# Kernel optimization log

Hardware: AMD Instinct MI355X
Metric: run time of the kernel (lower is better)

## Reference

```python
import jax, jax.numpy as jnp
import numpy as np

B, S, H, F, E, TOPK = 2, 2048, 1024, 512, 8, 2


def setup_inputs() -> dict:
    key = jax.random.key(0)
    k1, k2, k3, k4, k5 = jax.random.split(key, 5)
    s_h = 1.0 / np.sqrt(H)
    s_f = 1.0 / np.sqrt(F)
    return {
        "x": jax.random.normal(k1, (B, S, H), dtype=jnp.float32),
        "Wr": jax.random.normal(k2, (H, E), dtype=jnp.float32) * s_h,   # router
        "Wg": jax.random.normal(k3, (E, H, F), dtype=jnp.float32) * s_h,  # gate proj
        "Wu": jax.random.normal(k4, (E, H, F), dtype=jnp.float32) * s_h,  # up proj
        "Wd": jax.random.normal(k5, (E, F, H), dtype=jnp.float32) * s_f,  # down proj
        "topk": TOPK,
    }


def reference(x, Wr, Wg, Wu, Wd, topk):
    Bq, Sq, Hq = x.shape
    Eq = Wr.shape[1]
    xf = x.reshape(-1, Hq)                      # [T, H]
    logits = xf @ Wr                            # [T, E]
    probs = jax.nn.softmax(logits, axis=-1)
    w, idx = jax.lax.top_k(probs, topk)         # [T, topk]
    w = w / jnp.sum(w, axis=-1, keepdims=True)  # normalize top-k probs (Qwen3-style)
    # combine coefficients per (token, expert): scatter top-k weights
    coeff = jnp.sum(jax.nn.one_hot(idx, Eq, dtype=w.dtype) * w[..., None], axis=1)  # [T, E]
    # dense dispatch/combine (math-equivalent to per-expert gather + scatter-add)
    gate = jnp.einsum('th,ehf->tef', xf, Wg)    # [T, E, F]
    up = jnp.einsum('th,ehf->tef', xf, Wu)
    act = jax.nn.silu(gate) * up                # SwiGLU expert
    # apply combine weight before down-proj (linearity) to avoid a [T,E,H] temp
    out = jnp.einsum('tef,efh->th', act * coeff[:, :, None], Wd)
    return out.reshape(Bq, Sq, Hq)
```

## Files before the change

### kernel.cpp

```cpp
#include <hip/hip_runtime.h>
#include <hip/hip_bf16.h>

#define T_TOK    4096
#define H_DIM    1024
#define F_DIM    512
#define N_EXP    8
#define N_ASSIGN 8192
#define BM 128
#define BN 128
#define BK 64
#define MAX_TILES 80
#define GRID_MT   71
#define TRU      3072

typedef __bf16 bf16x8 __attribute__((ext_vector_type(8)));
typedef float  f32x4  __attribute__((ext_vector_type(4)));

#define MFMA16(a, b, c) __builtin_amdgcn_mfma_f32_16x16x32_bf16((a), (b), (c), 0, 0, 0)

__device__ __forceinline__ void gl_lds16(const __bf16* g, __bf16* l) {
    __builtin_amdgcn_global_load_lds(
        (const __attribute__((address_space(1))) unsigned int*)g,
        (__attribute__((address_space(3))) unsigned int*)l,
        16, 0, 0);
}

__global__ __launch_bounds__(256) void transpose_kernel(
    const float* __restrict__ Wg, const float* __restrict__ Wu, const float* __restrict__ Wd,
    __bf16* __restrict__ Wcat, __bf16* __restrict__ Wdt)
{
    __shared__ float tile[64][65];
    int b = blockIdx.x, tid = threadIdx.x;
    const float* src; int C, z, c0, r0;
    if (b < 2048) {
        z = b >> 7; int rem = b & 127;
        c0 = (rem & 7) * 64; r0 = (rem >> 3) * 64;
        src = (z < 8) ? Wg + (size_t)z * H_DIM * F_DIM
                      : Wu + (size_t)(z - 8) * H_DIM * F_DIM;
        C = F_DIM;
    } else {
        int v = b - 2048; z = 16 + (v >> 7); int rem = v & 127;
        c0 = (rem & 15) * 64; r0 = (rem >> 4) * 64;
        src = Wd + (size_t)(z - 16) * F_DIM * H_DIM;
        C = H_DIM;
    }
    int fr = tid >> 4, f4 = tid & 15;
#pragma unroll
    for (int p = 0; p < 4; ++p) {
        int row = p * 16 + fr;
        float4 v = *(const float4*)(src + (size_t)(r0 + row) * C + c0 + f4 * 4);
        tile[row][f4 * 4 + 0] = v.x; tile[row][f4 * 4 + 1] = v.y;
        tile[row][f4 * 4 + 2] = v.z; tile[row][f4 * 4 + 3] = v.w;
    }
    __syncthreads();
    int j = tid & 7, cl = tid >> 3;
#pragma unroll
    for (int p = 0; p < 2; ++p) {
        int c = cl + p * 32;
        bf16x8 v;
#pragma unroll
        for (int i = 0; i < 8; ++i) v[i] = (__bf16)tile[8 * j + i][c];
        if (z < 16) {
            int e = (z < 8) ? z : z - 8;
            int sel = (z < 8) ? 0 : 16;
            int f = c0 + c;
            int pp = ((f >> 4) << 5) + (f & 15) + sel;
            *(bf16x8*)&Wcat[(size_t)e * 2 * F_DIM * H_DIM + (size_t)pp * H_DIM + r0 + 8 * j] = v;
        } else {
            *(bf16x8*)&Wdt[(size_t)(z - 16) * H_DIM * F_DIM + (size_t)(c0 + c) * F_DIM + r0 + 8 * j] = v;
        }
    }
}

__global__ __launch_bounds__(256) void routing_kernel(
    const float* __restrict__ x, const float* __restrict__ Wr,
    __bf16* __restrict__ xb, int* __restrict__ top_e, float* __restrict__ top_w)
{
    __shared__ float WrS[N_EXP * H_DIM];
    int tid = threadIdx.x;
    for (int i = tid; i < N_EXP * H_DIM; i += 256) {
        int h = i >> 3, e = i & 7;
        WrS[e * H_DIM + (h ^ (e << 2))] = Wr[i];
    }
    __syncthreads();

    int wave = tid >> 6, lane = tid & 63;
    int t = blockIdx.x * 4 + wave;
    const float* xrow = x + (size_t)t * H_DIM;
    __bf16* xbrow = xb + (size_t)t * H_DIM;

    float part[N_EXP];
#pragma unroll
    for (int e = 0; e < N_EXP; ++e) part[e] = 0.f;
#pragma unroll 4
    for (int s = 0; s < 16; ++s) {
        int h = s * 64 + lane;
        float xs = xrow[h];
        xbrow[h] = (__bf16)xs;
#pragma unroll
        for (int e = 0; e < N_EXP; ++e) part[e] += xs * WrS[e * H_DIM + (h ^ (e << 2))];
    }
#pragma unroll
    for (int m = 1; m < 64; m <<= 1) {
#pragma unroll
        for (int e = 0; e < N_EXP; ++e) part[e] += __shfl_xor(part[e], m, 64);
    }
    if (lane == 0) {
        float v1 = -1e30f, v2 = -1e30f;
        int i1 = 0, i2 = 0;
#pragma unroll
        for (int e = 0; e < N_EXP; ++e) {
            float p = part[e];
            if (p > v1)      { v2 = v1; i2 = i1; v1 = p; i1 = e; }
            else if (p > v2) { v2 = p;  i2 = e; }
        }
        float w1 = 1.f / (1.f + __expf(v2 - v1));
        top_e[t * 2]     = i1;  top_e[t * 2 + 1] = i2;
        top_w[t * 2]     = w1;  top_w[t * 2 + 1] = 1.f - w1;
    }
}

__global__ __launch_bounds__(256) void sort_kernel(
    const int* __restrict__ top_e, const float* __restrict__ top_w,
    int* __restrict__ perm, float* __restrict__ wts, int* __restrict__ tokslot,
    int* __restrict__ tile_e, int* __restrict__ tile_m0, int* __restrict__ tile_cnt,
    int* __restrict__ n_tiles)
{
    __shared__ int hist[N_EXP][256];
    __shared__ int ebase[N_EXP];
    int tid = threadIdx.x, myexp = blockIdx.x;
    int c[N_EXP];
#pragma unroll
    for (int e = 0; e < N_EXP; ++e) c[e] = 0;
#pragma unroll 4
    for (int i = 0; i < 32; ++i) {
        int ee = top_e[i * 256 + tid];
#pragma unroll
        for (int e = 0; e < N_EXP; ++e) c[e] += (ee == e);
    }
#pragma unroll
    for (int e = 0; e < N_EXP; ++e) hist[e][tid] = c[e];
    __syncthreads();
    for (int s = 1; s < 256; s <<= 1) {
        int v[N_EXP];
#pragma unroll
        for (int e = 0; e < N_EXP; ++e) v[e] = (tid >= s) ? hist[e][tid - s] : 0;
        __syncthreads();
#pragma unroll
        for (int e = 0; e < N_EXP; ++e) hist[e][tid] += v[e];
        __syncthreads();
    }
    if (tid == 0) {
        int o = 0, nt = 0;
        for (int e = 0; e < N_EXP; ++e) {
            ebase[e] = o;
            int ne = hist[e][255];
            if (myexp == 0) {
                for (int m0 = 0; m0 < ne; m0 += BM) {
                    tile_e[nt]   = e;
                    tile_m0[nt]  = o + m0;
                    tile_cnt[nt] = (ne - m0 < BM) ? (ne - m0) : BM;
                    ++nt;
                }
            }
            o += ne;
        }
        if (myexp == 0) *n_tiles = nt;
    }
    __syncthreads();
    int base = ebase[myexp] + hist[myexp][tid] - c[myexp];
#pragma unroll 4
    for (int i = 0; i < 32; ++i) {
        int a = i * 256 + tid;
        if (top_e[a] == myexp) {
            perm[base]   = a >> 1;
            wts[base]    = top_w[a];
            tokslot[a]   = base;
            ++base;
        }
    }
}

__global__ __launch_bounds__(256, 3) void gateup_kernel(
    const __bf16* __restrict__ xb, const __bf16* __restrict__ Wcat,
    const int* __restrict__ perm, const float* __restrict__ wts,
    const int* __restrict__ tile_e, const int* __restrict__ tile_m0, const int* __restrict__ tile_cnt,
    const int* __restrict__ n_tiles, __bf16* __restrict__ act)
{
    int nat = (blockIdx.x & 7) * GRID_MT + (blockIdx.x >> 3);
    int mt = nat >> 3;
    if (mt >= *n_tiles) return;
    int e = tile_e[mt], m0 = tile_m0[mt], mcnt = tile_cnt[mt];
    int n0 = (nat & 7) * BN;
    __shared__ __align__(16) __bf16 As[BM * BK];
    __shared__ __align__(16) __bf16 Bs[BN * BK];
    __shared__ int   rowtok[BM];
    __shared__ float roww[BM];
    int tid = threadIdx.x;
    if (tid < BM) {
        int slot = m0 + ((tid < mcnt) ? tid : 0);
        rowtok[tid] = perm[slot];
        roww[tid]   = wts[slot];
    }
    __syncthreads();
    int wave = tid >> 6, lane = tid & 63;
    int srow   = wave * 8 + (lane >> 3);
    int schunk = (((lane & 7) ^ ((lane >> 3) & 7))) * 8;
    const __bf16* We = Wcat + (size_t)e * (2 * F_DIM) * H_DIM;
    const __bf16* aptr[4];
    const __bf16* bptr[4];
#pragma unroll
    for (int j = 0; j < 4; ++j) {
        int r = j * 32 + srow;
        aptr[j] = xb + (size_t)rowtok[r] * H_DIM + schunk;
        bptr[j] = We + (size_t)(n0 + r) * H_DIM + schunk;
    }
    __bf16* aLds = As + wave * 512;
    __bf16* bLds = Bs + wave * 512;
    int wm = wave & 1, wn = wave >> 1;
    int quad = lane >> 4, l16 = lane & 15;
    f32x4 acc[4][4];
#pragma unroll
    for (int a = 0; a < 4; ++a)
#pragma unroll
        for (int b = 0; b < 4; ++b) acc[a][b] = (f32x4){0.f, 0.f, 0.f, 0.f};
    for (int k0 = 0; k0 < H_DIM; k0 += BK) {
#pragma unroll
        for (int j = 0; j < 4; ++j) {
            gl_lds16(aptr[j] + k0, aLds + j * 2048);
            gl_lds16(bptr[j] + k0, bLds + j * 2048);
        }
        __syncthreads();
#pragma unroll
        for (int s = 0; s < 2; ++s) {
            int sw = (((quad + s * 4) ^ (l16 & 7))) * 8;
            bf16x8 af[4], bf[4];
#pragma unroll
            for (int im = 0; im < 4; ++im)
                af[im] = *(const bf16x8*)&As[(wm * 64 + im * 16 + l16) * 64 + sw];
#pragma unroll
            for (int in = 0; in < 4; ++in)
                bf[in] = *(const bf16x8*)&Bs[(wn * 64 + in * 16 + l16) * 64 + sw];
#pragma unroll
            for (int im = 0; im < 4; ++im)
#pragma unroll
                for (int in = 0; in < 4; ++in)
                    acc[im][in] = MFMA16(af[im], bf[in], acc[im][in]);
        }
        __syncthreads();
    }
    int fbase = (n0 >> 1) + wn * 32;
#pragma unroll
    for (int im = 0; im < 4; ++im) {
#pragma unroll
        for (int ip = 0; ip < 2; ++ip) {
            f32x4 g = acc[im][ip * 2], u = acc[im][ip * 2 + 1];
            int fcol = fbase + ip * 16 + l16;
#pragma unroll
            for (int r = 0; r < 4; ++r) {
                int rl = wm * 64 + im * 16 + quad * 4 + r;
                if (rl < mcnt) {
                    float gv = g[r], uv = u[r];
                    float sg = gv / (1.f + __expf(-gv));
                    act[(size_t)(m0 + rl) * F_DIM + fcol] = (__bf16)(sg * uv * roww[rl]);
                }
            }
        }
    }
}

__global__ __launch_bounds__(256, 3) void down_kernel(
    const __bf16* __restrict__ act, const __bf16* __restrict__ Wdt,
    const int* __restrict__ tile_e, const int* __restrict__ tile_m0, const int* __restrict__ tile_cnt,
    const int* __restrict__ n_tiles, __bf16* __restrict__ P)
{
    int nat = (blockIdx.x & 7) * GRID_MT + (blockIdx.x >> 3);
    int mt = nat >> 3;
    if (mt >= *n_tiles) return;
    int e = tile_e[mt], m0 = tile_m0[mt], mcnt = tile_cnt[mt];
    int n0 = (nat & 7) * BN;
    __shared__ __align__(16) __bf16 As[BM * BK];
    __shared__ __align__(16) __bf16 Bs[BN * BK];
    int tid = threadIdx.x;
    int wave = tid >> 6, lane = tid & 63;
    int srow   = wave * 8 + (lane >> 3);
    int schunk = (((lane & 7) ^ ((lane >> 3) & 7))) * 8;
    const __bf16* Wd_e = Wdt + (size_t)e * H_DIM * F_DIM;
    const __bf16* aptr[4];
    const __bf16* bptr[4];
#pragma unroll
    for (int j = 0; j < 4; ++j) {
        int r = j * 32 + srow;
        int ar = m0 + ((r < mcnt) ? r : 0);
        aptr[j] = act  + (size_t)ar * F_DIM + schunk;
        bptr[j] = Wd_e + (size_t)(n0 + r) * F_DIM + schunk;
    }
    __bf16* aLds = As + wave * 512;
    __bf16* bLds = Bs + wave * 512;
    int wm = wave & 1, wn = wave >> 1;
    int quad = lane >> 4, l16 = lane & 15;
    f32x4 acc[4][4];
#pragma unroll
    for (int a = 0; a < 4; ++a)
#pragma unroll
        for (int b = 0; b < 4; ++b) acc[a][b] = (f32x4){0.f, 0.f, 0.f, 0.f};
    for (int k0 = 0; k0 < F_DIM; k0 += BK) {
#pragma unroll
        for (int j = 0; j < 4; ++j) {
            gl_lds16(aptr[j] + k0, aLds + j * 2048);
            gl_lds16(bptr[j] + k0, bLds + j * 2048);
        }
        __syncthreads();
#pragma unroll
        for (int s = 0; s < 2; ++s) {
            int sw = (((quad + s * 4) ^ (l16 & 7))) * 8;
            bf16x8 af[4], bf[4];
#pragma unroll
            for (int im = 0; im < 4; ++im)
                af[im] = *(const bf16x8*)&As[(wm * 64 + im * 16 + l16) * 64 + sw];
#pragma unroll
            for (int in = 0; in < 4; ++in)
                bf[in] = *(const bf16x8*)&Bs[(wn * 64 + in * 16 + l16) * 64 + sw];
#pragma unroll
            for (int im = 0; im < 4; ++im)
#pragma unroll
                for (int in = 0; in < 4; ++in)
                    acc[im][in] = MFMA16(af[im], bf[in], acc[im][in]);
        }
        __syncthreads();
    }
#pragma unroll
    for (int im = 0; im < 4; ++im) {
#pragma unroll
        for (int in = 0; in < 4; ++in) {
            int col = n0 + wn * 64 + in * 16 + l16;
#pragma unroll
            for (int r = 0; r < 4; ++r) {
                int rl = wm * 64 + im * 16 + quad * 4 + r;
                if (rl < mcnt)
                    P[(size_t)(m0 + rl) * H_DIM + col] = (__bf16)acc[im][in][r];
            }
        }
    }
}

__global__ __launch_bounds__(256) void combine_kernel(
    const __bf16* __restrict__ P, const int* __restrict__ tokslot,
    float* __restrict__ out)
{
    int wave = threadIdx.x >> 6, lane = threadIdx.x & 63;
    int t = blockIdx.x * 4 + wave;
    int s1 = tokslot[2 * t], s2 = tokslot[2 * t + 1];
    const bf16x8* p1 = (const bf16x8*)(P + (size_t)s1 * H_DIM);
    const bf16x8* p2 = (const bf16x8*)(P + (size_t)s2 * H_DIM);
    float* o = out + (size_t)t * H_DIM;
#pragma unroll
    for (int i = 0; i < 2; ++i) {
        int idx = i * 64 + lane;
        bf16x8 a = p1[idx], b = p2[idx];
        f32x4 lo, hi;
#pragma unroll
        for (int j = 0; j < 4; ++j) lo[j] = (float)a[j] + (float)b[j];
#pragma unroll
        for (int j = 0; j < 4; ++j) hi[j] = (float)a[4 + j] + (float)b[4 + j];
        *(f32x4*)(o + idx * 8)     = lo;
        *(f32x4*)(o + idx * 8 + 4) = hi;
    }
}

extern "C" void kernel_launch(void* const* d_in, const int* in_sizes, int n_in,
                              void* d_out, int out_size, void* d_ws, size_t ws_size,
                              hipStream_t stream)
{
    const float* x  = (const float*)d_in[0];
    const float* Wr = (const float*)d_in[1];
    const float* Wg = (const float*)d_in[2];
    const float* Wu = (const float*)d_in[3];
    const float* Wd = (const float*)d_in[4];
    float* out = (float*)d_out;

    char* ws = (char*)d_ws;
    size_t off = 0;
    auto carve = [&](size_t bytes) {
        char* p = ws + off;
        off = (off + bytes + 255) & ~(size_t)255;
        return p;
    };
    __bf16* xb   = (__bf16*)carve((size_t)T_TOK * H_DIM * 2);
    __bf16* Wcat = (__bf16*)carve((size_t)N_EXP * 2 * F_DIM * H_DIM * 2);
    __bf16* Wdt  = (__bf16*)carve((size_t)N_EXP * H_DIM * F_DIM * 2);
    __bf16* act  = (__bf16*)carve((size_t)N_ASSIGN * F_DIM * 2);
    __bf16* P    = (__bf16*)carve((size_t)N_ASSIGN * H_DIM * 2);
    int*   top_e = (int*)carve((size_t)T_TOK * 2 * sizeof(int));
    float* top_w = (float*)carve((size_t)T_TOK * 2 * sizeof(float));
    int*   perm  = (int*)carve((size_t)N_ASSIGN * sizeof(int));
    float* wts   = (float*)carve((size_t)N_ASSIGN * sizeof(float));
    int*  tokslot= (int*)carve((size_t)N_ASSIGN * sizeof(int));
    int*   tl_e  = (int*)carve(MAX_TILES * sizeof(int));
    int*   tl_m0 = (int*)carve(MAX_TILES * sizeof(int));
    int*   tl_cn = (int*)carve(MAX_TILES * sizeof(int));
    int*   n_til = (int*)carve(sizeof(int));

    transpose_kernel<<<TRU, 256, 0, stream>>>(Wg, Wu, Wd, Wcat, Wdt);
    routing_kernel<<<T_TOK / 4, 256, 0, stream>>>(x, Wr, xb, top_e, top_w);
    sort_kernel<<<N_EXP, 256, 0, stream>>>(
        top_e, top_w, perm, wts, tokslot, tl_e, tl_m0, tl_cn, n_til);
    gateup_kernel<<<GRID_MT * 8, 256, 0, stream>>>(
        xb, Wcat, perm, wts, tl_e, tl_m0, tl_cn, n_til, act);
    down_kernel<<<GRID_MT * 8, 256, 0, stream>>>(
        act, Wdt, tl_e, tl_m0, tl_cn, n_til, P);
    combine_kernel<<<T_TOK / 4, 256, 0, stream>>>(P, tokslot, out);
}
```

Before: 184.6 us.

## Triple-buffer LDS tiles with BK=32 in gate-up and down GEMM kernels

Both grouped GEMM kernels now use a three-stage ring of LDS buffers holding 32-wide K slices, prefetching two slices ahead with direct global-to-LDS loads. Each iteration waits on the vmcnt counter and issues one barrier instead of two, so global loads overlap with MFMA work rather than stalling on every tile. The swizzle changes to fit 32-element rows. Risks: each iteration does half the MFMA work, so barrier overhead per FLOP doubles. The hand-written waitcnt/barrier sequencing must be exactly right, and LDS use grows 1.5x, which may limit the 3-blocks-per-CU occupancy.

```diff
diff --git a/kernel.cpp b/kernel.cpp
--- a/kernel.cpp
+++ b/kernel.cpp
@@ -8,7 +8,7 @@
 #define N_ASSIGN 8192
 #define BM 128
 #define BN 128
-#define BK 64
+#define BK32 32
 #define MAX_TILES 80
 #define GRID_MT   71
 #define TRU      3072
@@ -192,8 +192,8 @@
     if (mt >= *n_tiles) return;
     int e = tile_e[mt], m0 = tile_m0[mt], mcnt = tile_cnt[mt];
     int n0 = (nat & 7) * BN;
-    __shared__ __align__(16) __bf16 As[BM * BK];
-    __shared__ __align__(16) __bf16 Bs[BN * BK];
+    __shared__ __align__(16) __bf16 As[3][BM * BK32];
+    __shared__ __align__(16) __bf16 Bs[3][BN * BK32];
     __shared__ int   rowtok[BM];
     __shared__ float roww[BM];
     int tid = threadIdx.x;
@@ -204,51 +204,60 @@
     }
     __syncthreads();
     int wave = tid >> 6, lane = tid & 63;
-    int srow   = wave * 8 + (lane >> 3);
-    int schunk = (((lane & 7) ^ ((lane >> 3) & 7))) * 8;
+    int srow = lane >> 2;
+    int g8   = ((lane & 3) ^ ((lane >> 3) & 3)) * 8;
     const __bf16* We = Wcat + (size_t)e * (2 * F_DIM) * H_DIM;
-    const __bf16* aptr[4];
-    const __bf16* bptr[4];
-#pragma unroll
-    for (int j = 0; j < 4; ++j) {
-        int r = j * 32 + srow;
-        aptr[j] = xb + (size_t)rowtok[r] * H_DIM + schunk;
-        bptr[j] = We + (size_t)(n0 + r) * H_DIM + schunk;
-    }
-    __bf16* aLds = As + wave * 512;
-    __bf16* bLds = Bs + wave * 512;
+    const __bf16* aps[2];
+    const __bf16* bps[2];
+#pragma unroll
+    for (int j = 0; j < 2; ++j) {
+        int r = wave * 32 + j * 16 + srow;
+        aps[j] = xb + (size_t)rowtok[r] * H_DIM + g8;
+        bps[j] = We + (size_t)(n0 + r) * H_DIM + g8;
+    }
+#define STAGE_GU(Ab, Bb, kk) do {                                         \
+        _Pragma("unroll")                                                 \
+        for (int j = 0; j < 2; ++j) {                                     \
+            gl_lds16(aps[j] + (kk), (Ab) + (wave * 32 + j * 16) * BK32);  \
+            gl_lds16(bps[j] + (kk), (Bb) + (wave * 32 + j * 16) * BK32);  \
+        }                                                                 \
+    } while (0)
+    __bf16 *A0 = As[0], *A1 = As[1], *A2 = As[2];
+    __bf16 *B0 = Bs[0], *B1 = Bs[1], *B2 = Bs[2];
     int wm = wave & 1, wn = wave >> 1;
     int quad = lane >> 4, l16 = lane & 15;
+    int rsw = (quad ^ ((l16 >> 1) & 3)) * 8;
     f32x4 acc[4][4];
 #pragma unroll
     for (int a = 0; a < 4; ++a)
 #pragma unroll
         for (int b = 0; b < 4; ++b) acc[a][b] = (f32x4){0.f, 0.f, 0.f, 0.f};
-    for (int k0 = 0; k0 < H_DIM; k0 += BK) {
-#pragma unroll
-        for (int j = 0; j < 4; ++j) {
-            gl_lds16(aptr[j] + k0, aLds + j * 2048);
-            gl_lds16(bptr[j] + k0, bLds + j * 2048);
-        }
-        __syncthreads();
-#pragma unroll
-        for (int s = 0; s < 2; ++s) {
-            int sw = (((quad + s * 4) ^ (l16 & 7))) * 8;
-            bf16x8 af[4], bf[4];
-#pragma unroll
-            for (int im = 0; im < 4; ++im)
-                af[im] = *(const bf16x8*)&As[(wm * 64 + im * 16 + l16) * 64 + sw];
+
+    STAGE_GU(A0, B0, 0);
+    STAGE_GU(A1, B1, BK32);
+    const int NT = H_DIM / BK32;
+    for (int t = 0; t < NT; ++t) {
+        if (t + 1 < NT) asm volatile("s_waitcnt vmcnt(4)" ::: "memory");
+        else            asm volatile("s_waitcnt vmcnt(0)" ::: "memory");
+        asm volatile("s_barrier" ::: "memory");
+        if (t + 2 < NT) STAGE_GU(A2, B2, (t + 2) * BK32);
+        bf16x8 af[4], bf[4];
+#pragma unroll
+        for (int im = 0; im < 4; ++im)
+            af[im] = *(const bf16x8*)&A0[(wm * 64 + im * 16 + l16) * BK32 + rsw];
+#pragma unroll
+        for (int in = 0; in < 4; ++in)
+            bf[in] = *(const bf16x8*)&B0[(wn * 64 + in * 16 + l16) * BK32 + rsw];
+#pragma unroll
+        for (int im = 0; im < 4; ++im)
 #pragma unroll
             for (int in = 0; in < 4; ++in)
-                bf[in] = *(const bf16x8*)&Bs[(wn * 64 + in * 16 + l16) * 64 + sw];
-#pragma unroll
-            for (int im = 0; im < 4; ++im)
-#pragma unroll
-                for (int in = 0; in < 4; ++in)
-                    acc[im][in] = MFMA16(af[im], bf[in], acc[im][in]);
-        }
-        __syncthreads();
-    }
+                acc[im][in] = MFMA16(af[im], bf[in], acc[im][in]);
+        __bf16* tp;
+        tp = A0; A0 = A1; A1 = A2; A2 = tp;
+        tp = B0; B0 = B1; B1 = B2; B2 = tp;
+    }
+#undef STAGE_GU
     int fbase = (n0 >> 1) + wn * 32;
 #pragma unroll
     for (int im = 0; im < 4; ++im) {
@@ -279,56 +288,65 @@
     if (mt >= *n_tiles) return;
     int e = tile_e[mt], m0 = tile_m0[mt], mcnt = tile_cnt[mt];
     int n0 = (nat & 7) * BN;
-    __shared__ __align__(16) __bf16 As[BM * BK];
-    __shared__ __align__(16) __bf16 Bs[BN * BK];
+    __shared__ __align__(16) __bf16 As[3][BM * BK32];
+    __shared__ __align__(16) __bf16 Bs[3][BN * BK32];
     int tid = threadIdx.x;
     int wave = tid >> 6, lane = tid & 63;
-    int srow   = wave * 8 + (lane >> 3);
-    int schunk = (((lane & 7) ^ ((lane >> 3) & 7))) * 8;
+    int srow = lane >> 2;
+    int g8   = ((lane & 3) ^ ((lane >> 3) & 3)) * 8;
     const __bf16* Wd_e = Wdt + (size_t)e * H_DIM * F_DIM;
-    const __bf16* aptr[4];
-    const __bf16* bptr[4];
-#pragma unroll
-    for (int j = 0; j < 4; ++j) {
-        int r = j * 32 + srow;
+    const __bf16* aps[2];
+    const __bf16* bps[2];
+#pragma unroll
+    for (int j = 0; j < 2; ++j) {
+        int r = wave * 32 + j * 16 + srow;
         int ar = m0 + ((r < mcnt) ? r : 0);
-        aptr[j] = act  + (size_t)ar * F_DIM + schunk;
-        bptr[j] = Wd_e + (size_t)(n0 + r) * F_DIM + schunk;
-    }
-    __bf16* aLds = As + wave * 512;
-    __bf16* bLds = Bs + wave * 512;
+        aps[j] = act  + (size_t)ar * F_DIM + g8;
+        bps[j] = Wd_e + (size_t)(n0 + r) * F_DIM + g8;
+    }
+#define STAGE_DN(Ab, Bb, kk) do {                                         \
+        _Pragma("unroll")                                                 \
+        for (int j = 0; j < 2; ++j) {                                     \
+            gl_lds16(aps[j] + (kk), (Ab) + (wave * 32 + j * 16) * BK32);  \
+            gl_lds16(bps[j] + (kk), (Bb) + (wave * 32 + j * 16) * BK32);  \
+        }                                                                 \
+    } while (0)
+    __bf16 *A0 = As[0], *A1 = As[1], *A2 = As[2];
+    __bf16 *B0 = Bs[0], *B1 = Bs[1], *B2 = Bs[2];
     int wm = wave & 1, wn = wave >> 1;
     int quad = lane >> 4, l16 = lane & 15;
+    int rsw = (quad ^ ((l16 >> 1) & 3)) * 8;
     f32x4 acc[4][4];
 #pragma unroll
     for (int a = 0; a < 4; ++a)
 #pragma unroll
         for (int b = 0; b < 4; ++b) acc[a][b] = (f32x4){0.f, 0.f, 0.f, 0.f};
-    for (int k0 = 0; k0 < F_DIM; k0 += BK) {
-#pragma unroll
-        for (int j = 0; j < 4; ++j) {
-            gl_lds16(aptr[j] + k0, aLds + j * 2048);
-            gl_lds16(bptr[j] + k0, bLds + j * 2048);
-        }
-        __syncthreads();
-#pragma unroll
-        for (int s = 0; s < 2; ++s) {
-            int sw = (((quad + s * 4) ^ (l16 & 7))) * 8;
-            bf16x8 af[4], bf[4];
-#pragma unroll
-            for (int im = 0; im < 4; ++im)
-                af[im] = *(const bf16x8*)&As[(wm * 64 + im * 16 + l16) * 64 + sw];
+
+    STAGE_DN(A0, B0, 0);
+    STAGE_DN(A1, B1, BK32);
+    const int NT = F_DIM / BK32;
+    for (int t = 0; t < NT; ++t) {
+        if (t + 1 < NT) asm volatile("s_waitcnt vmcnt(4)" ::: "memory");
+        else            asm volatile("s_waitcnt vmcnt(0)" ::: "memory");
+        asm volatile("s_barrier" ::: "memory");
+        if (t + 2 < NT) STAGE_DN(A2, B2, (t + 2) * BK32);
+        bf16x8 af[4], bf[4];
+#pragma unroll
+        for (int im = 0; im < 4; ++im)
+            af[im] = *(const bf16x8*)&A0[(wm * 64 + im * 16 + l16) * BK32 + rsw];
+#pragma unroll
+        for (int in = 0; in < 4; ++in)
+            bf[in] = *(const bf16x8*)&B0[(wn * 64 + in * 16 + l16) * BK32 + rsw];
+#pragma unroll
+        for (int im = 0; im < 4; ++im)
 #pragma unroll
             for (int in = 0; in < 4; ++in)
-                bf[in] = *(const bf16x8*)&Bs[(wn * 64 + in * 16 + l16) * 64 + sw];
-#pragma unroll
-            for (int im = 0; im < 4; ++im)
-#pragma unroll
-                for (int in = 0; in < 4; ++in)
-                    acc[im][in] = MFMA16(af[im], bf[in], acc[im][in]);
-        }
-        __syncthreads();
-    }
+                acc[im][in] = MFMA16(af[im], bf[in], acc[im][in]);
+        __bf16* tp;
+        tp = A0; A0 = A1; A1 = A2; A2 = tp;
+        tp = B0; B0 = B1; B1 = B2; B2 = tp;
+    }
+#undef STAGE_DN
 #pragma unroll
     for (int im = 0; im < 4; ++im) {
 #pragma unroll
```

Result: slower. 192.7 us (+4.4%).

## Fuse gate-up and down GEMMs into one kernel with per-tile ready counters

Applied to the files above, without the earlier changes.

Merges the gate/up SwiGLU GEMM and the down-projection GEMM into a single kernel. Each block computes its slice of act, signals an atomic per-M-tile counter, then spins until all 8 N-blocks of that tile have finished before running the down GEMM on the same tile. This removes one kernel launch and the global barrier between the stages. The cost is spin-waiting, and there is a deadlock risk if co-resident blocks cannot cover all sibling blocks (568 blocks at occupancy 3 on 256 CUs should fit).

```diff
diff --git a/kernel.cpp b/kernel.cpp
--- a/kernel.cpp
+++ b/kernel.cpp
@@ -124,11 +124,12 @@
     const int* __restrict__ top_e, const float* __restrict__ top_w,
     int* __restrict__ perm, float* __restrict__ wts, int* __restrict__ tokslot,
     int* __restrict__ tile_e, int* __restrict__ tile_m0, int* __restrict__ tile_cnt,
-    int* __restrict__ n_tiles)
+    int* __restrict__ n_tiles, int* __restrict__ rdy)
 {
     __shared__ int hist[N_EXP][256];
     __shared__ int ebase[N_EXP];
     int tid = threadIdx.x, myexp = blockIdx.x;
+    if (myexp == 0 && tid < MAX_TILES) rdy[tid] = 0;
     int c[N_EXP];
 #pragma unroll
     for (int e = 0; e < N_EXP; ++e) c[e] = 0;
@@ -181,11 +182,13 @@
     }
 }
 
-__global__ __launch_bounds__(256, 3) void gateup_kernel(
+__global__ __launch_bounds__(256, 3) void fused_gemm_kernel(
     const __bf16* __restrict__ xb, const __bf16* __restrict__ Wcat,
+    const __bf16* __restrict__ Wdt,
     const int* __restrict__ perm, const float* __restrict__ wts,
     const int* __restrict__ tile_e, const int* __restrict__ tile_m0, const int* __restrict__ tile_cnt,
-    const int* __restrict__ n_tiles, __bf16* __restrict__ act)
+    const int* __restrict__ n_tiles, __bf16* __restrict__ act,
+    __bf16* __restrict__ P, int* __restrict__ rdy)
 {
     int nat = (blockIdx.x & 7) * GRID_MT + (blockIdx.x >> 3);
     int mt = nat >> 3;
@@ -206,139 +209,137 @@
     int wave = tid >> 6, lane = tid & 63;
     int srow   = wave * 8 + (lane >> 3);
     int schunk = (((lane & 7) ^ ((lane >> 3) & 7))) * 8;
-    const __bf16* We = Wcat + (size_t)e * (2 * F_DIM) * H_DIM;
-    const __bf16* aptr[4];
-    const __bf16* bptr[4];
-#pragma unroll
-    for (int j = 0; j < 4; ++j) {
-        int r = j * 32 + srow;
-        aptr[j] = xb + (size_t)rowtok[r] * H_DIM + schunk;
-        bptr[j] = We + (size_t)(n0 + r) * H_DIM + schunk;
-    }
+    int wm = wave & 1, wn = wave >> 1;
+    int quad = lane >> 4, l16 = lane & 15;
     __bf16* aLds = As + wave * 512;
     __bf16* bLds = Bs + wave * 512;
-    int wm = wave & 1, wn = wave >> 1;
-    int quad = lane >> 4, l16 = lane & 15;
-    f32x4 acc[4][4];
-#pragma unroll
-    for (int a = 0; a < 4; ++a)
-#pragma unroll
-        for (int b = 0; b < 4; ++b) acc[a][b] = (f32x4){0.f, 0.f, 0.f, 0.f};
-    for (int k0 = 0; k0 < H_DIM; k0 += BK) {
+
+    {
+        const __bf16* We = Wcat + (size_t)e * (2 * F_DIM) * H_DIM;
+        const __bf16* aptr[4];
+        const __bf16* bptr[4];
 #pragma unroll
         for (int j = 0; j < 4; ++j) {
-            gl_lds16(aptr[j] + k0, aLds + j * 2048);
-            gl_lds16(bptr[j] + k0, bLds + j * 2048);
-        }
-        __syncthreads();
-#pragma unroll
-        for (int s = 0; s < 2; ++s) {
-            int sw = (((quad + s * 4) ^ (l16 & 7))) * 8;
-            bf16x8 af[4], bf[4];
-#pragma unroll
-            for (int im = 0; im < 4; ++im)
-                af[im] = *(const bf16x8*)&As[(wm * 64 + im * 16 + l16) * 64 + sw];
-#pragma unroll
-            for (int in = 0; in < 4; ++in)
-                bf[in] = *(const bf16x8*)&Bs[(wn * 64 + in * 16 + l16) * 64 + sw];
-#pragma unroll
-            for (int im = 0; im < 4; ++im)
+            int r = j * 32 + srow;
+            aptr[j] = xb + (size_t)rowtok[r] * H_DIM + schunk;
+            bptr[j] = We + (size_t)(n0 + r) * H_DIM + schunk;
+        }
+        f32x4 acc[4][4];
+#pragma unroll
+        for (int a = 0; a < 4; ++a)
+#pragma unroll
+            for (int b = 0; b < 4; ++b) acc[a][b] = (f32x4){0.f, 0.f, 0.f, 0.f};
+        for (int k0 = 0; k0 < H_DIM; k0 += BK) {
+#pragma unroll
+            for (int j = 0; j < 4; ++j) {
+                gl_lds16(aptr[j] + k0, aLds + j * 2048);
+                gl_lds16(bptr[j] + k0, bLds + j * 2048);
+            }
+            __syncthreads();
+#pragma unroll
+            for (int s = 0; s < 2; ++s) {
+                int sw = (((quad + s * 4) ^ (l16 & 7))) * 8;
+                bf16x8 af[4], bf[4];
+#pragma unroll
+                for (int im = 0; im < 4; ++im)
+                    af[im] = *(const bf16x8*)&As[(wm * 64 + im * 16 + l16) * 64 + sw];
 #pragma unroll
                 for (int in = 0; in < 4; ++in)
-                    acc[im][in] = MFMA16(af[im], bf[in], acc[im][in]);
-        }
-        __syncthreads();
-    }
-    int fbase = (n0 >> 1) + wn * 32;
-#pragma unroll
-    for (int im = 0; im < 4; ++im) {
-#pragma unroll
-        for (int ip = 0; ip < 2; ++ip) {
-            f32x4 g = acc[im][ip * 2], u = acc[im][ip * 2 + 1];
-            int fcol = fbase + ip * 16 + l16;
-#pragma unroll
-            for (int r = 0; r < 4; ++r) {
-                int rl = wm * 64 + im * 16 + quad * 4 + r;
-                if (rl < mcnt) {
-                    float gv = g[r], uv = u[r];
-                    float sg = gv / (1.f + __expf(-gv));
-                    act[(size_t)(m0 + rl) * F_DIM + fcol] = (__bf16)(sg * uv * roww[rl]);
+                    bf[in] = *(const bf16x8*)&Bs[(wn * 64 + in * 16 + l16) * 64 + sw];
+#pragma unroll
+                for (int im = 0; im < 4; ++im)
+#pragma unroll
+                    for (int in = 0; in < 4; ++in)
+                        acc[im][in] = MFMA16(af[im], bf[in], acc[im][in]);
+            }
+            __syncthreads();
+        }
+        int fbase = (n0 >> 1) + wn * 32;
+#pragma unroll
+        for (int im = 0; im < 4; ++im) {
+#pragma unroll
+            for (int ip = 0; ip < 2; ++ip) {
+                f32x4 g = acc[im][ip * 2], u = acc[im][ip * 2 + 1];
+                int fcol = fbase + ip * 16 + l16;
+#pragma unroll
+                for (int r = 0; r < 4; ++r) {
+                    int rl = wm * 64 + im * 16 + quad * 4 + r;
+                    if (rl < mcnt) {
+                        float gv = g[r], uv = u[r];
+                        float sg = gv / (1.f + __expf(-gv));
+                        act[(size_t)(m0 + rl) * F_DIM + fcol] = (__bf16)(sg * uv * roww[rl]);
+                    }
                 }
             }
         }
     }
-}
-
-__global__ __launch_bounds__(256, 3) void down_kernel(
-    const __bf16* __restrict__ act, const __bf16* __restrict__ Wdt,
-    const int* __restrict__ tile_e, const int* __restrict__ tile_m0, const int* __restrict__ tile_cnt,
-    const int* __restrict__ n_tiles, __bf16* __restrict__ P)
-{
-    int nat = (blockIdx.x & 7) * GRID_MT + (blockIdx.x >> 3);
-    int mt = nat >> 3;
-    if (mt >= *n_tiles) return;
-    int e = tile_e[mt], m0 = tile_m0[mt], mcnt = tile_cnt[mt];
-    int n0 = (nat & 7) * BN;
-    __shared__ __align__(16) __bf16 As[BM * BK];
-    __shared__ __align__(16) __bf16 Bs[BN * BK];
-    int tid = threadIdx.x;
-    int wave = tid >> 6, lane = tid & 63;
-    int srow   = wave * 8 + (lane >> 3);
-    int schunk = (((lane & 7) ^ ((lane >> 3) & 7))) * 8;
-    const __bf16* Wd_e = Wdt + (size_t)e * H_DIM * F_DIM;
-    const __bf16* aptr[4];
-    const __bf16* bptr[4];
-#pragma unroll
-    for (int j = 0; j < 4; ++j) {
-        int r = j * 32 + srow;
-        int ar = m0 + ((r < mcnt) ? r : 0);
-        aptr[j] = act  + (size_t)ar * F_DIM + schunk;
-        bptr[j] = Wd_e + (size_t)(n0 + r) * F_DIM + schunk;
-    }
-    __bf16* aLds = As + wave * 512;
-    __bf16* bLds = Bs + wave * 512;
-    int wm = wave & 1, wn = wave >> 1;
-    int quad = lane >> 4, l16 = lane & 15;
-    f32x4 acc[4][4];
-#pragma unroll
-    for (int a = 0; a < 4; ++a)
-#pragma unroll
-        for (int b = 0; b < 4; ++b) acc[a][b] = (f32x4){0.f, 0.f, 0.f, 0.f};
-    for (int k0 = 0; k0 < F_DIM; k0 += BK) {
+
+    __threadfence();
+    __syncthreads();
+    if (tid == 0)
+        __hip_atomic_fetch_add(&rdy[mt], 1, __ATOMIC_RELAXED,
+                               __HIP_MEMORY_SCOPE_AGENT);
+
+    if (tid == 0) {
+        while (__hip_atomic_load(&rdy[mt], __ATOMIC_RELAXED,
+                                 __HIP_MEMORY_SCOPE_AGENT) < 8)
+            __builtin_amdgcn_s_sleep(2);
+    }
+    __syncthreads();
+    __threadfence();
+
+    {
+        const __bf16* Wd_e = Wdt + (size_t)e * H_DIM * F_DIM;
+        const __bf16* aptr[4];
+        const __bf16* bptr[4];
 #pragma unroll
         for (int j = 0; j < 4; ++j) {
-            gl_lds16(aptr[j] + k0, aLds + j * 2048);
-            gl_lds16(bptr[j] + k0, bLds + j * 2048);
-        }
-        __syncthreads();
-#pragma unroll
-        for (int s = 0; s < 2; ++s) {
-            int sw = (((quad + s * 4) ^ (l16 & 7))) * 8;
-            bf16x8 af[4], bf[4];
-#pragma unroll
-            for (int im = 0; im < 4; ++im)
-                af[im] = *(const bf16x8*)&As[(wm * 64 + im * 16 + l16) * 64 + sw];
-#pragma unroll
-            for (int in = 0; in < 4; ++in)
-                bf[in] = *(const bf16x8*)&Bs[(wn * 64 + in * 16 + l16) * 64 + sw];
-#pragma unroll
-            for (int im = 0; im < 4; ++im)
+            int r = j * 32 + srow;
+            int ar = m0 + ((r < mcnt) ? r : 0);
+            aptr[j] = act  + (size_t)ar * F_DIM + schunk;
+            bptr[j] = Wd_e + (size_t)(n0 + r) * F_DIM + schunk;
+        }
+        f32x4 acc[4][4];
+#pragma unroll
+        for (int a = 0; a < 4; ++a)
+#pragma unroll
+            for (int b = 0; b < 4; ++b) acc[a][b] = (f32x4){0.f, 0.f, 0.f, 0.f};
+        for (int k0 = 0; k0 < F_DIM; k0 += BK) {
+#pragma unroll
+            for (int j = 0; j < 4; ++j) {
+                gl_lds16(aptr[j] + k0, aLds + j * 2048);
+                gl_lds16(bptr[j] + k0, bLds + j * 2048);
+            }
+            __syncthreads();
+#pragma unroll
+            for (int s = 0; s < 2; ++s) {
+                int sw = (((quad + s * 4) ^ (l16 & 7))) * 8;
+                bf16x8 af[4], bf[4];
+#pragma unroll
+                for (int im = 0; im < 4; ++im)
+                    af[im] = *(const bf16x8*)&As[(wm * 64 + im * 16 + l16) * 64 + sw];
 #pragma unroll
                 for (int in = 0; in < 4; ++in)
-                    acc[im][in] = MFMA16(af[im], bf[in], acc[im][in]);
-        }
-        __syncthreads();
-    }
-#pragma unroll
-    for (int im = 0; im < 4; ++im) {
-#pragma unroll
-        for (int in = 0; in < 4; ++in) {
-            int col = n0 + wn * 64 + in * 16 + l16;
-#pragma unroll
-            for (int r = 0; r < 4; ++r) {
-                int rl = wm * 64 + im * 16 + quad * 4 + r;
-                if (rl < mcnt)
-                    P[(size_t)(m0 + rl) * H_DIM + col] = (__bf16)acc[im][in][r];
+                    bf[in] = *(const bf16x8*)&Bs[(wn * 64 + in * 16 + l16) * 64 + sw];
+#pragma unroll
+                for (int im = 0; im < 4; ++im)
+#pragma unroll
+                    for (int in = 0; in < 4; ++in)
+                        acc[im][in] = MFMA16(af[im], bf[in], acc[im][in]);
+            }
+            __syncthreads();
+        }
+#pragma unroll
+        for (int im = 0; im < 4; ++im) {
+#pragma unroll
+            for (int in = 0; in < 4; ++in) {
+                int col = n0 + wn * 64 + in * 16 + l16;
+#pragma unroll
+                for (int r = 0; r < 4; ++r) {
+                    int rl = wm * 64 + im * 16 + quad * 4 + r;
+                    if (rl < mcnt)
+                        P[(size_t)(m0 + rl) * H_DIM + col] = (__bf16)acc[im][in][r];
+                }
             }
         }
     }
@@ -400,14 +401,13 @@
     int*   tl_m0 = (int*)carve(MAX_TILES * sizeof(int));
     int*   tl_cn = (int*)carve(MAX_TILES * sizeof(int));
     int*   n_til = (int*)carve(sizeof(int));
+    int*   rdy   = (int*)carve(MAX_TILES * sizeof(int));
 
     transpose_kernel<<<TRU, 256, 0, stream>>>(Wg, Wu, Wd, Wcat, Wdt);
     routing_kernel<<<T_TOK / 4, 256, 0, stream>>>(x, Wr, xb, top_e, top_w);
     sort_kernel<<<N_EXP, 256, 0, stream>>>(
-        top_e, top_w, perm, wts, tokslot, tl_e, tl_m0, tl_cn, n_til);
-    gateup_kernel<<<GRID_MT * 8, 256, 0, stream>>>(
-        xb, Wcat, perm, wts, tl_e, tl_m0, tl_cn, n_til, act);
-    down_kernel<<<GRID_MT * 8, 256, 0, stream>>>(
-        act, Wdt, tl_e, tl_m0, tl_cn, n_til, P);
+        top_e, top_w, perm, wts, tokslot, tl_e, tl_m0, tl_cn, n_til, rdy);
+    fused_gemm_kernel<<<GRID_MT * 8, 256, 0, stream>>>(
+        xb, Wcat, Wdt, perm, wts, tl_e, tl_m0, tl_cn, n_til, act, P, rdy);
     combine_kernel<<<T_TOK / 4, 256, 0, stream>>>(P, tokslot, out);
 }
```

Result: slower. 318.9 us (+72.7%).
